# Optimization experiments

Measured on AMD Instinct MI355X. Metric: run time of the kernel, lower is better.

## Reference

```python
import jax, jax.numpy as jnp
import numpy as np

B, S, H, A, O = 512, 64, 1024, 1024, 1024
ATT = 64  # attention logit width (== encoder seq len)


def setup_inputs() -> dict:
    key = jax.random.key(0)
    ks = jax.random.split(key, 14)
    s = lambda *sh: 1.0 / np.sqrt(sh[-1])
    return {
        "encoder_outputs": jax.random.normal(ks[0], (B, S, A), jnp.float32),
        "hidden": jax.random.normal(ks[1], (1, B, H), jnp.float32),
        "max_length": 128,
        # attention: Linear(H+O -> 64)
        "Wa": jax.random.normal(ks[2], (ATT, H + O), jnp.float32) * s(H + O),
        "ba": jnp.zeros((ATT,), jnp.float32),
        # attention_combine: Linear(A+O -> H)
        "Wc": jax.random.normal(ks[3], (H, A + O), jnp.float32) * s(A + O),
        "bc": jnp.zeros((H,), jnp.float32),
        # GRU (1 layer): weight_ih [3H,H], weight_hh [3H,H]
        "W_ih": jax.random.normal(ks[4], (3 * H, H), jnp.float32) * s(H),
        "W_hh": jax.random.normal(ks[5], (3 * H, H), jnp.float32) * s(H),
        "b_ih": jnp.zeros((3 * H,), jnp.float32),
        "b_hh": jnp.zeros((3 * H,), jnp.float32),
        # fc_out: Linear(H -> O)
        "Wo": jax.random.normal(ks[6], (O, H), jnp.float32) * s(H),
        "bo": jnp.zeros((O,), jnp.float32),
    }


def _decode(encoder_outputs, h0, max_length, Wa, ba, Wc, bc, W_ih, W_hh, b_ih, b_hh, Wo, bo):
    Hs = h0.shape[-1]
    dec0 = jnp.zeros((encoder_outputs.shape[0], Wo.shape[0]), encoder_outputs.dtype)

    def step(carry, _):
        dec_in, h = carry  # [B,O], [B,H]
        temp = jnp.concatenate([dec_in, h], axis=1)  # [B, O+H]... matches cat(dec, hidden[-1])
        attn_w = jax.nn.softmax(temp @ Wa.T + ba, axis=1)  # [B,64]
        attn_applied = jnp.einsum("bs,bsd->bd", attn_w, encoder_outputs)  # [B,A]
        gru_in = jax.nn.relu(jnp.concatenate([dec_in, attn_applied], axis=1) @ Wc.T + bc)  # [B,H]
        # single-step PyTorch GRU cell
        gi = gru_in @ W_ih.T + b_ih  # [B,3H]
        gh = h @ W_hh.T + b_hh
        r = jax.nn.sigmoid(gi[:, :Hs] + gh[:, :Hs])
        z = jax.nn.sigmoid(gi[:, Hs:2 * Hs] + gh[:, Hs:2 * Hs])
        n = jnp.tanh(gi[:, 2 * Hs:] + r * gh[:, 2 * Hs:])
        h_new = (1.0 - z) * n + z * h
        out_tok = h_new @ Wo.T + bo  # [B,O]
        return (out_tok, h_new), out_tok

    (_, h_fin), outs = jax.lax.scan(step, (dec0, h0[0]), None, length=max_length)
    output_seq = jnp.transpose(outs, (1, 0, 2))  # [B,T,O]
    return output_seq, h_fin[None]


def reference(encoder_outputs, hidden, max_length, Wa, ba, Wc, bc, W_ih, W_hh, b_ih, b_hh, Wo, bo):
    return _decode(encoder_outputs, hidden, max_length, Wa, ba, Wc, bc, W_ih, W_hh, b_ih, b_hh, Wo, bo)
```

## Files before the change

### kernel.cpp

```cpp
#include <hip/hip_runtime.h>
#include <hip/hip_bf16.h>

#define B 512
#define S 64
#define H 1024
#define O 1024
#define T 128
#define ATT 64

typedef __bf16 bf16;
typedef __bf16 bf16x8 __attribute__((ext_vector_type(8)));
typedef __bf16 bf16x4 __attribute__((ext_vector_type(4)));
typedef float f32x4 __attribute__((ext_vector_type(4)));

static __device__ __forceinline__ float bf2f(bf16 b) {
    unsigned short s = __builtin_bit_cast(unsigned short, b);
    unsigned int u = ((unsigned int)s) << 16;
    return __builtin_bit_cast(float, u);
}
static __device__ __forceinline__ bf16 f2bf(float f) {
    unsigned int u = __builtin_bit_cast(unsigned int, f);
    unsigned int r = (u + 0x7fffu + ((u >> 16) & 1u)) >> 16;
    return __builtin_bit_cast(bf16, (unsigned short)r);
}

template <bool RELU, int K, int SPLITK, int KSTART>
__global__ __launch_bounds__(256) void gemm_kernel(
    const bf16* __restrict__ A0, long lda0,
    const bf16* __restrict__ A1, long lda1,
    const bf16* __restrict__ W, const float* __restrict__ bias,
    float* __restrict__ Cf, long ldc, bf16* __restrict__ Cbf, int ldcbf) {
    const int tid = threadIdx.x;
    const int wave = tid >> 6, lane = tid & 63;
    const int wm = wave >> 1, wn = wave & 1;
    const int quad = lane >> 4, r = lane & 15;
    const int kq = quad * 8;

    const int m0 = blockIdx.y * 32 + wm * 16 + r;
    const int n0 = blockIdx.x * 64 + wn * 32;

    const bf16* a0row = A0 + (long)m0 * lda0;
    const bf16* a1row = A1 + (long)m0 * lda1;
    const bf16* w0 = W + (long)(n0 + r) * K;
    const bf16* w1 = W + (long)(n0 + 16 + r) * K;

    f32x4 acc0 = {0.f, 0.f, 0.f, 0.f}, acc1 = {0.f, 0.f, 0.f, 0.f};

    for (int k0 = KSTART; k0 < K; k0 += 32) {
        bf16x8 av;
        if (k0 < SPLITK)
            av = *(const bf16x8*)(a0row + k0 + kq);
        else
            av = *(const bf16x8*)(a1row + (k0 - SPLITK) + kq);
        bf16x8 bv0 = *(const bf16x8*)(w0 + k0 + kq);
        bf16x8 bv1 = *(const bf16x8*)(w1 + k0 + kq);
        acc0 = __builtin_amdgcn_mfma_f32_16x16x32_bf16(av, bv0, acc0, 0, 0, 0);
        acc1 = __builtin_amdgcn_mfma_f32_16x16x32_bf16(av, bv1, acc1, 0, 0, 0);
    }

    const int mbase = blockIdx.y * 32 + wm * 16 + quad * 4;
    const int nA = n0 + r, nB = n0 + 16 + r;
    const float biasA = bias[nA], biasB = bias[nB];
#pragma unroll
    for (int reg = 0; reg < 4; ++reg) {
        const int m = mbase + reg;
        float vA = acc0[reg] + biasA;
        float vB = acc1[reg] + biasB;
        if (RELU) { vA = fmaxf(vA, 0.f); vB = fmaxf(vB, 0.f); }
        if (Cf) {
            Cf[(long)m * ldc + nA] = vA;
            Cf[(long)m * ldc + nB] = vB;
        }
        if (Cbf) {
            Cbf[(long)m * ldcbf + nA] = f2bf(vA);
            Cbf[(long)m * ldcbf + nB] = f2bf(vB);
        }
    }
}

__global__ __launch_bounds__(256) void fcout_batch_kernel(
    const bf16* __restrict__ Hh, const bf16* __restrict__ Wo,
    const float* __restrict__ bo, float* __restrict__ out) {
    const int tid = threadIdx.x;
    const int wave = tid >> 6, lane = tid & 63;
    const int wm = wave >> 1, wn = wave & 1;
    const int quad = lane >> 4, r = lane & 15;
    const int kq = quad * 8;

    const int m0 = blockIdx.y * 32 + wm * 16 + r;
    const int n0 = blockIdx.x * 64 + wn * 32;

    const bf16* arow = Hh + (long)m0 * H;
    const bf16* w0 = Wo + (long)(n0 + r) * H;
    const bf16* w1 = Wo + (long)(n0 + 16 + r) * H;

    f32x4 acc0 = {0.f, 0.f, 0.f, 0.f}, acc1 = {0.f, 0.f, 0.f, 0.f};
    for (int k0 = 0; k0 < H; k0 += 32) {
        bf16x8 av = *(const bf16x8*)(arow + k0 + kq);
        bf16x8 bv0 = *(const bf16x8*)(w0 + k0 + kq);
        bf16x8 bv1 = *(const bf16x8*)(w1 + k0 + kq);
        acc0 = __builtin_amdgcn_mfma_f32_16x16x32_bf16(av, bv0, acc0, 0, 0, 0);
        acc1 = __builtin_amdgcn_mfma_f32_16x16x32_bf16(av, bv1, acc1, 0, 0, 0);
    }

    const int mbase = blockIdx.y * 32 + wm * 16 + quad * 4;
    const int nA = n0 + r, nB = n0 + 16 + r;
    const float biasA = bo[nA], biasB = bo[nB];
#pragma unroll
    for (int reg = 0; reg < 4; ++reg) {
        const int m = mbase + reg;
        const int b = m & (B - 1);
        const int tt = m >> 9;
        float* orow = out + (long)b * ((long)T * O) + (long)tt * O;
        orow[nA] = acc0[reg] + biasA;
        orow[nB] = acc1[reg] + biasB;
    }
}

__global__ __launch_bounds__(256) void attn_logits_kernel(
    const bf16* __restrict__ h, const bf16* __restrict__ Wlog,
    const float* __restrict__ bvec, bf16* __restrict__ attn_w) {
    __shared__ float lg[32][64];
    const int tid = threadIdx.x;
    const int wave = tid >> 6, lane = tid & 63;
    const int wm = wave >> 1, wn = wave & 1;
    const int quad = lane >> 4, r = lane & 15;
    const int kq = quad * 8;

    const int m0 = blockIdx.y * 32 + wm * 16 + r;
    const int n0 = wn * 32;

    const bf16* hrow = h + (long)m0 * H;
    const bf16* w0 = Wlog + (long)(n0 + r) * H;
    const bf16* w1 = Wlog + (long)(n0 + 16 + r) * H;

    f32x4 acc0 = {0.f, 0.f, 0.f, 0.f}, acc1 = {0.f, 0.f, 0.f, 0.f};
    for (int k0 = 0; k0 < H; k0 += 32) {
        bf16x8 av = *(const bf16x8*)(hrow + k0 + kq);
        bf16x8 bv0 = *(const bf16x8*)(w0 + k0 + kq);
        bf16x8 bv1 = *(const bf16x8*)(w1 + k0 + kq);
        acc0 = __builtin_amdgcn_mfma_f32_16x16x32_bf16(av, bv0, acc0, 0, 0, 0);
        acc1 = __builtin_amdgcn_mfma_f32_16x16x32_bf16(av, bv1, acc1, 0, 0, 0);
    }

    const int mloc = wm * 16 + quad * 4;
#pragma unroll
    for (int reg = 0; reg < 4; ++reg) {
        lg[mloc + reg][n0 + r] = acc0[reg] + bvec[n0 + r];
        lg[mloc + reg][n0 + 16 + r] = acc1[reg] + bvec[n0 + 16 + r];
    }
    __syncthreads();

    if (tid < 32) {
        const int row = tid;
        float mx = -1e30f;
#pragma unroll
        for (int s = 0; s < 64; ++s) mx = fmaxf(mx, lg[row][s]);
        float sum = 0.f;
#pragma unroll
        for (int s = 0; s < 64; ++s) sum += __expf(lg[row][s] - mx);
        const float inv = 1.f / sum;
        const long gb = (long)(blockIdx.y * 32 + row) * 64;
#pragma unroll
        for (int s = 0; s < 64; ++s)
            attn_w[gb + s] = f2bf(__expf(lg[row][s] - mx) * inv);
    }
}

__global__ __launch_bounds__(256) void attn_apply_kernel(
    const bf16* __restrict__ attn_w, const bf16* __restrict__ enc,
    bf16* __restrict__ attn_out) {
    __shared__ float w[64];
    const int b = blockIdx.x;
    const int tid = threadIdx.x;
    if (tid < 64) w[tid] = bf2f(attn_w[b * 64 + tid]);
    __syncthreads();
    const bf16* e = enc + (long)b * (S * 1024) + tid * 4;
    float a0 = 0.f, a1 = 0.f, a2 = 0.f, a3 = 0.f;
#pragma unroll 16
    for (int s = 0; s < S; ++s) {
        unsigned long long raw =
            __builtin_nontemporal_load((const unsigned long long*)(e + (long)s * 1024));
        bf16x4 v = __builtin_bit_cast(bf16x4, raw);
        const float ws = w[s];
        a0 += ws * bf2f(v[0]);
        a1 += ws * bf2f(v[1]);
        a2 += ws * bf2f(v[2]);
        a3 += ws * bf2f(v[3]);
    }
    bf16x4 o = {f2bf(a0), f2bf(a1), f2bf(a2), f2bf(a3)};
    *(bf16x4*)(attn_out + (long)b * 1024 + tid * 4) = o;
}

__global__ __launch_bounds__(256) void gru_kernel(
    const bf16* __restrict__ gin, const bf16* __restrict__ hbf,
    const bf16* __restrict__ Wih, const bf16* __restrict__ Whh,
    const float* __restrict__ bih, const float* __restrict__ bhh,
    const float* __restrict__ hold, float* __restrict__ hnew,
    bf16* __restrict__ hnewbf) {
    const int tid = threadIdx.x;
    const int wave = tid >> 6, lane = tid & 63;
    const int wm = wave >> 1, wn = wave & 1;
    const int quad = lane >> 4, r = lane & 15;
    const int kq = quad * 8;

    const int m0 = blockIdx.y * 32 + wm * 16 + r;
    const int n0 = blockIdx.x * 64 + wn * 32;

    const bf16* grow = gin + (long)m0 * H;
    const bf16* hrow = hbf + (long)m0 * H;

    const bf16* wi[3][2];
    const bf16* wh[3][2];
#pragma unroll
    for (int g = 0; g < 3; ++g) {
#pragma unroll
        for (int ni = 0; ni < 2; ++ni) {
            const long row = (long)g * H + n0 + ni * 16 + r;
            wi[g][ni] = Wih + row * H;
            wh[g][ni] = Whh + row * H;
        }
    }

    f32x4 aI[3][2], aH[3][2];
#pragma unroll
    for (int g = 0; g < 3; ++g)
#pragma unroll
        for (int ni = 0; ni < 2; ++ni) {
            aI[g][ni] = (f32x4){0.f, 0.f, 0.f, 0.f};
            aH[g][ni] = (f32x4){0.f, 0.f, 0.f, 0.f};
        }

    for (int k0 = 0; k0 < H; k0 += 32) {
        const int ko = k0 + kq;
        bf16x8 ai = *(const bf16x8*)(grow + ko);
        bf16x8 ah = *(const bf16x8*)(hrow + ko);
#pragma unroll
        for (int g = 0; g < 3; ++g) {
#pragma unroll
            for (int ni = 0; ni < 2; ++ni) {
                bf16x8 bi = *(const bf16x8*)(wi[g][ni] + ko);
                aI[g][ni] = __builtin_amdgcn_mfma_f32_16x16x32_bf16(ai, bi, aI[g][ni], 0, 0, 0);
                bf16x8 bh = *(const bf16x8*)(wh[g][ni] + ko);
                aH[g][ni] = __builtin_amdgcn_mfma_f32_16x16x32_bf16(ah, bh, aH[g][ni], 0, 0, 0);
            }
        }
    }

    const int mbase = blockIdx.y * 32 + wm * 16 + quad * 4;
#pragma unroll
    for (int ni = 0; ni < 2; ++ni) {
        const int j = n0 + ni * 16 + r;
        const float bir = bih[j], biz = bih[j + H], bin = bih[j + 2 * H];
        const float bhr = bhh[j], bhz = bhh[j + H], bhn = bhh[j + 2 * H];
#pragma unroll
        for (int reg = 0; reg < 4; ++reg) {
            const int m = mbase + reg;
            const float gir = aI[0][ni][reg] + bir, ghr = aH[0][ni][reg] + bhr;
            const float giz = aI[1][ni][reg] + biz, ghz = aH[1][ni][reg] + bhz;
            const float ginv = aI[2][ni][reg] + bin, ghn = aH[2][ni][reg] + bhn;
            const float rg = 1.f / (1.f + __expf(-(gir + ghr)));
            const float zg = 1.f / (1.f + __expf(-(giz + ghz)));
            const float ng = tanhf(ginv + rg * ghn);
            const long idx = (long)m * H + j;
            const float hv = hold[idx];
            const float hnv = (1.f - zg) * ng + zg * hv;
            hnew[idx] = hnv;
            hnewbf[idx] = f2bf(hnv);
        }
    }
}

__global__ __launch_bounds__(256) void cast2d_kernel(
    const float* __restrict__ src, long ld_src, long soff,
    bf16* __restrict__ dst, long ld_dst, long doff, long rows, long cols4) {
    const long total = rows * cols4;
    const long stride = (long)gridDim.x * blockDim.x;
    for (long i = (long)blockIdx.x * blockDim.x + threadIdx.x; i < total; i += stride) {
        const long rr = i / cols4;
        const long c = (i - rr * cols4) << 2;
        const float4 v = *(const float4*)(src + rr * ld_src + soff + c);
        bf16x4 o = {f2bf(v.x), f2bf(v.y), f2bf(v.z), f2bf(v.w)};
        *(bf16x4*)(dst + rr * ld_dst + doff + c) = o;
    }
}

__global__ __launch_bounds__(256) void transpose_cast_kernel(
    const float* __restrict__ src, bf16* __restrict__ dst, int n) {
    __shared__ float tile[32][33];
    const int tx = threadIdx.x & 31, ty = threadIdx.x >> 5;
    const int x0 = blockIdx.x * 32, y0 = blockIdx.y * 32;
#pragma unroll
    for (int i = 0; i < 32; i += 8)
        tile[ty + i][tx] = src[(long)(y0 + ty + i) * n + x0 + tx];
    __syncthreads();
#pragma unroll
    for (int i = 0; i < 32; i += 8)
        dst[(long)(x0 + ty + i) * n + y0 + tx] = f2bf(tile[tx][ty + i]);
}

__global__ __launch_bounds__(256) void addcast_wlog_kernel(
    const float* __restrict__ P1, const float* __restrict__ Wa,
    bf16* __restrict__ Wlog1) {
    const int i = blockIdx.x * 256 + threadIdx.x;
    if (i < 64 * 1024) {
        const int rr = i >> 10, c = i & 1023;
        Wlog1[i] = f2bf(P1[i] + Wa[(long)rr * 2048 + 1024 + c]);
    }
}

__global__ __launch_bounds__(256) void bias_fuse_kernel(
    const float* __restrict__ W, long ld, const float* __restrict__ v,
    const float* __restrict__ b_in, float* __restrict__ b_out) {
    __shared__ float red[256];
    const int r = blockIdx.x, tid = threadIdx.x;
    float s = 0.f;
    for (int j = tid; j < 1024; j += 256) s += W[(long)r * ld + j] * v[j];
    red[tid] = s;
    __syncthreads();
    for (int off = 128; off > 0; off >>= 1) {
        if (tid < off) red[tid] += red[tid + off];
        __syncthreads();
    }
    if (tid == 0) b_out[r] = b_in[r] + red[0];
}

__global__ __launch_bounds__(256) void init_h_kernel(
    const float* __restrict__ h0, float* __restrict__ hfp,
    bf16* __restrict__ hbf, long n4) {
    long i = (long)blockIdx.x * blockDim.x + threadIdx.x;
    const long stride = (long)gridDim.x * blockDim.x;
    for (; i < n4; i += stride) {
        float4 v = ((const float4*)h0)[i];
        ((float4*)hfp)[i] = v;
        bf16x4 o = {f2bf(v.x), f2bf(v.y), f2bf(v.z), f2bf(v.w)};
        *(bf16x4*)(hbf + 4 * i) = o;
    }
}

__global__ __launch_bounds__(256) void copy_f32_kernel(
    const float* __restrict__ src, float* __restrict__ dst, long n4) {
    long i = (long)blockIdx.x * blockDim.x + threadIdx.x;
    const long stride = (long)gridDim.x * blockDim.x;
    for (; i < n4; i += stride) ((float4*)dst)[i] = ((const float4*)src)[i];
}

extern "C" void kernel_launch(void* const* d_in, const int* in_sizes, int n_in,
                              void* d_out, int out_size, void* d_ws, size_t ws_size,
                              hipStream_t stream) {
    const float* enc_f = (const float*)d_in[0];
    const float* hidden = (const float*)d_in[1];
    const float* Wa = (const float*)d_in[3];
    const float* ba = (const float*)d_in[4];
    const float* Wc = (const float*)d_in[5];
    const float* bc = (const float*)d_in[6];
    const float* Wih = (const float*)d_in[7];
    const float* Whh = (const float*)d_in[8];
    const float* bih = (const float*)d_in[9];
    const float* bhh = (const float*)d_in[10];
    const float* Wo = (const float*)d_in[11];
    const float* bo = (const float*)d_in[12];
    float* out = (float*)d_out;

    char* p = (char*)d_ws;
    auto carve = [&](long bytes) {
        char* q = p;
        p += (bytes + 255) & ~255L;
        return q;
    };
    bf16* Wlog0 = (bf16*)carve((long)64 * 1024 * 2);
    bf16* Wlog1 = (bf16*)carve((long)64 * 1024 * 2);
    bf16* Wcomb = (bf16*)carve((long)H * 2048 * 2);
    bf16* Wih_bf = (bf16*)carve((long)3 * H * H * 2);
    bf16* Whh_bf = (bf16*)carve((long)3 * H * H * 2);
    bf16* Wo_bf = (bf16*)carve((long)O * H * 2);
    bf16* enc_bf = (bf16*)carve((long)B * S * 1024 * 2);
    bf16* attn_bf = (bf16*)carve((long)B * 1024 * 2);
    bf16* gru_bf = (bf16*)carve((long)B * H * 2);
    bf16* attn_w = (bf16*)carve((long)B * 64 * 2);
    bf16* h0bf = (bf16*)carve((long)B * H * 2);
    bf16* hbfA = (bf16*)carve((long)B * H * 2);
    bf16* hbfB = (bf16*)carve((long)B * H * 2);
    float* hfpA = (float*)carve((long)B * H * 4);
    float* hfpB = (float*)carve((long)B * H * 4);
    float* blog1 = (float*)carve(64 * 4);
    float* bc2 = (float*)carve((long)H * 4);
    float* zeros = (float*)carve(1024 * 4);

    const long persistent = (long)(p - (char*)d_ws);
    const long histBytes = (long)T * B * H * 2;
    const bool batched = (ws_size >= (size_t)(persistent + histBytes + 256));
    bf16* hist = batched ? (bf16*)carve(histBytes) : nullptr;
    auto slot = [&](int t2) -> bf16* {
        return batched ? hist + (long)t2 * ((long)B * H)
                       : ((t2 & 1) ? hbfB : hbfA);
    };

    {
        char* sp = (char*)enc_bf;
        auto scarve = [&](long bytes) {
            char* q = sp;
            sp += (bytes + 255) & ~255L;
            return q;
        };
        bf16* Wad = (bf16*)scarve((long)64 * 1024 * 2);
        bf16* Wcd = (bf16*)scarve((long)H * 1024 * 2);
        bf16* WoT = (bf16*)scarve((long)H * O * 2);
        float* P1 = (float*)scarve((long)64 * 1024 * 4);
        float* P2 = (float*)scarve((long)H * 1024 * 4);

        hipMemsetAsync(zeros, 0, 1024 * 4, stream);

        auto cast2d = [&](const float* src, long lds_, long so, bf16* dst,
                          long ldd, long doff, long rows, long cols) {
            long n4 = rows * (cols / 4);
            int blocks = (int)((n4 + 255) / 256);
            if (blocks > 4096) blocks = 4096;
            cast2d_kernel<<<blocks, 256, 0, stream>>>(src, lds_, so, dst, ldd,
                                                      doff, rows, cols / 4);
        };
        cast2d(Wa, 2048, 1024, Wlog0, 1024, 0, 64, 1024);
        cast2d(Wa, 2048, 0, Wad, 1024, 0, 64, 1024);
        cast2d(Wc, 2048, 0, Wcd, 1024, 0, 1024, 1024);
        cast2d(Wc, 2048, 1024, Wcomb, 2048, 1024, 1024, 1024);
        cast2d(Wih, 1024, 0, Wih_bf, 1024, 0, 3 * H, 1024);
        cast2d(Whh, 1024, 0, Whh_bf, 1024, 0, 3 * H, 1024);
        cast2d(Wo, 1024, 0, Wo_bf, 1024, 0, O, 1024);
        transpose_cast_kernel<<<dim3(32, 32), 256, 0, stream>>>(Wo, WoT, 1024);

        gemm_kernel<false, 1024, 1024, 0><<<dim3(16, 2), 256, 0, stream>>>(
            Wad, 1024, Wad, 1024, WoT, zeros, P1, 1024, nullptr, 0);
        gemm_kernel<false, 1024, 1024, 0><<<dim3(16, 32), 256, 0, stream>>>(
            Wcd, 1024, Wcd, 1024, WoT, zeros, P2, 1024, nullptr, 0);

        addcast_wlog_kernel<<<256, 256, 0, stream>>>(P1, Wa, Wlog1);
        cast2d(P2, 1024, 0, Wcomb, 2048, 0, 1024, 1024);

        bias_fuse_kernel<<<64, 256, 0, stream>>>(Wa, 2048, bo, ba, blog1);
        bias_fuse_kernel<<<1024, 256, 0, stream>>>(Wc, 2048, bo, bc, bc2);

        cast2d(enc_f, 1024, 0, enc_bf, 1024, 0, (long)B * S, 1024);
        init_h_kernel<<<512, 256, 0, stream>>>(hidden, hfpA, h0bf, (long)B * H / 4);
    }

    const dim3 blk(256);
    const dim3 grid_nm(H / 64, B / 32);
    const dim3 grid_attn(1, B / 32);

    for (int t = 0; t < T; ++t) {
        const bf16* h_in = (t == 0) ? h0bf : slot(t - 1);
        bf16* h_out = slot(t);
        const float* hfp_r = (t & 1) ? hfpB : hfpA;
        float* hfp_w = (t & 1) ? hfpA : hfpB;

        attn_logits_kernel<<<grid_attn, blk, 0, stream>>>(
            h_in, t ? Wlog1 : Wlog0, t ? blog1 : ba, attn_w);
        attn_apply_kernel<<<B, blk, 0, stream>>>(attn_w, enc_bf, attn_bf);
        if (t == 0)
            gemm_kernel<true, 2048, 1024, 1024><<<grid_nm, blk, 0, stream>>>(
                h_in, 1024, attn_bf, 1024, Wcomb, bc, nullptr, 0, gru_bf, H);
        else
            gemm_kernel<true, 2048, 1024, 0><<<grid_nm, blk, 0, stream>>>(
                h_in, 1024, attn_bf, 1024, Wcomb, bc2, nullptr, 0, gru_bf, H);
        gru_kernel<<<grid_nm, blk, 0, stream>>>(
            gru_bf, h_in, Wih_bf, Whh_bf, bih, bhh, hfp_r, hfp_w, h_out);
        if (!batched)
            gemm_kernel<false, 1024, 1024, 0><<<grid_nm, blk, 0, stream>>>(
                h_out, 1024, h_out, 1024, Wo_bf, bo,
                out + (long)t * O, (long)T * O, nullptr, 0);
    }

    if (batched)
        fcout_batch_kernel<<<dim3(16, (T * B) / 32), blk, 0, stream>>>(
            hist, Wo_bf, bo, out);

    copy_f32_kernel<<<512, 256, 0, stream>>>(hfpA, out + (long)B * T * O,
                                             (long)B * H / 4);
}
```

Baseline: 15.48 ms.

## Fuse attention logits/softmax into apply kernel and halve GEMM/GRU tile width

Merges the attention-logit GEMM plus softmax into the per-batch attention-apply kernel. Each block now computes its 64 logits with scalar dot products from an LDS-staged hidden row, which removes one launch and the attn_w round trip per step. The combine GEMM and GRU kernels drop from 64 to 32 output columns per block, doubling the grid to 512 blocks to raise occupancy on the many CUs. In exchange, A-row reloads increase and each block does less MFMA work per load.

```diff
diff --git a/kernel.cpp b/kernel.cpp
--- a/kernel.cpp
+++ b/kernel.cpp
@@ -78,6 +78,50 @@
     }
 }
 
+template <bool RELU, int K, int SPLITK, int KSTART>
+__global__ __launch_bounds__(256) void gemm32_kernel(
+    const bf16* __restrict__ A0, long lda0,
+    const bf16* __restrict__ A1, long lda1,
+    const bf16* __restrict__ W, const float* __restrict__ bias,
+    float* __restrict__ Cf, long ldc, bf16* __restrict__ Cbf, int ldcbf) {
+    const int tid = threadIdx.x;
+    const int wave = tid >> 6, lane = tid & 63;
+    const int wm = wave >> 1, wn = wave & 1;
+    const int quad = lane >> 4, r = lane & 15;
+    const int kq = quad * 8;
+
+    const int m0 = blockIdx.y * 32 + wm * 16 + r;
+    const int n0 = blockIdx.x * 32 + wn * 16;
+
+    const bf16* a0row = A0 + (long)m0 * lda0;
+    const bf16* a1row = A1 + (long)m0 * lda1;
+    const bf16* w0 = W + (long)(n0 + r) * K;
+
+    f32x4 acc0 = {0.f, 0.f, 0.f, 0.f};
+
+    for (int k0 = KSTART; k0 < K; k0 += 32) {
+        bf16x8 av;
+        if (k0 < SPLITK)
+            av = *(const bf16x8*)(a0row + k0 + kq);
+        else
+            av = *(const bf16x8*)(a1row + (k0 - SPLITK) + kq);
+        bf16x8 bv0 = *(const bf16x8*)(w0 + k0 + kq);
+        acc0 = __builtin_amdgcn_mfma_f32_16x16x32_bf16(av, bv0, acc0, 0, 0, 0);
+    }
+
+    const int mbase = blockIdx.y * 32 + wm * 16 + quad * 4;
+    const int nA = n0 + r;
+    const float biasA = bias[nA];
+#pragma unroll
+    for (int reg = 0; reg < 4; ++reg) {
+        const int m = mbase + reg;
+        float vA = acc0[reg] + biasA;
+        if (RELU) vA = fmaxf(vA, 0.f);
+        if (Cf) Cf[(long)m * ldc + nA] = vA;
+        if (Cbf) Cbf[(long)m * ldcbf + nA] = f2bf(vA);
+    }
+}
+
 __global__ __launch_bounds__(256) void fcout_batch_kernel(
     const bf16* __restrict__ Hh, const bf16* __restrict__ Wo,
     const float* __restrict__ bo, float* __restrict__ out) {
@@ -117,72 +161,67 @@
     }
 }
 
-__global__ __launch_bounds__(256) void attn_logits_kernel(
+#define HIDX(k) ((k) + (((k) >> 8) << 2))
+__global__ __launch_bounds__(256) void attn_fused_kernel(
     const bf16* __restrict__ h, const bf16* __restrict__ Wlog,
-    const float* __restrict__ bvec, bf16* __restrict__ attn_w) {
-    __shared__ float lg[32][64];
-    const int tid = threadIdx.x;
-    const int wave = tid >> 6, lane = tid & 63;
-    const int wm = wave >> 1, wn = wave & 1;
-    const int quad = lane >> 4, r = lane & 15;
-    const int kq = quad * 8;
-
-    const int m0 = blockIdx.y * 32 + wm * 16 + r;
-    const int n0 = wn * 32;
-
-    const bf16* hrow = h + (long)m0 * H;
-    const bf16* w0 = Wlog + (long)(n0 + r) * H;
-    const bf16* w1 = Wlog + (long)(n0 + 16 + r) * H;
-
-    f32x4 acc0 = {0.f, 0.f, 0.f, 0.f}, acc1 = {0.f, 0.f, 0.f, 0.f};
-    for (int k0 = 0; k0 < H; k0 += 32) {
-        bf16x8 av = *(const bf16x8*)(hrow + k0 + kq);
-        bf16x8 bv0 = *(const bf16x8*)(w0 + k0 + kq);
-        bf16x8 bv1 = *(const bf16x8*)(w1 + k0 + kq);
-        acc0 = __builtin_amdgcn_mfma_f32_16x16x32_bf16(av, bv0, acc0, 0, 0, 0);
-        acc1 = __builtin_amdgcn_mfma_f32_16x16x32_bf16(av, bv1, acc1, 0, 0, 0);
-    }
-
-    const int mloc = wm * 16 + quad * 4;
-#pragma unroll
-    for (int reg = 0; reg < 4; ++reg) {
-        lg[mloc + reg][n0 + r] = acc0[reg] + bvec[n0 + r];
-        lg[mloc + reg][n0 + 16 + r] = acc1[reg] + bvec[n0 + 16 + r];
-    }
-    __syncthreads();
-
-    if (tid < 32) {
-        const int row = tid;
-        float mx = -1e30f;
-#pragma unroll
-        for (int s = 0; s < 64; ++s) mx = fmaxf(mx, lg[row][s]);
-        float sum = 0.f;
-#pragma unroll
-        for (int s = 0; s < 64; ++s) sum += __expf(lg[row][s] - mx);
-        const float inv = 1.f / sum;
-        const long gb = (long)(blockIdx.y * 32 + row) * 64;
-#pragma unroll
-        for (int s = 0; s < 64; ++s)
-            attn_w[gb + s] = f2bf(__expf(lg[row][s] - mx) * inv);
-    }
-}
-
-__global__ __launch_bounds__(256) void attn_apply_kernel(
-    const bf16* __restrict__ attn_w, const bf16* __restrict__ enc,
+    const float* __restrict__ bvec, const bf16* __restrict__ enc,
     bf16* __restrict__ attn_out) {
-    __shared__ float w[64];
+    __shared__ float hsh[1040];
+    __shared__ float lg[64];
+    __shared__ float wbuf[64];
     const int b = blockIdx.x;
     const int tid = threadIdx.x;
-    if (tid < 64) w[tid] = bf2f(attn_w[b * 64 + tid]);
+
+    {
+        const int k = tid * 4;
+        bf16x4 v = *(const bf16x4*)(h + (long)b * H + k);
+        float4 f = {bf2f(v[0]), bf2f(v[1]), bf2f(v[2]), bf2f(v[3])};
+        *(float4*)&hsh[HIDX(k)] = f;
+    }
     __syncthreads();
+
+    {
+        const int s = tid >> 2, kpart = tid & 3;
+        const bf16* wrow = Wlog + (long)s * 1024 + kpart * 256;
+        const int kb = kpart * 256;
+        float acc = 0.f;
+#pragma unroll
+        for (int i = 0; i < 32; ++i) {
+            bf16x8 wv = *(const bf16x8*)(wrow + i * 8);
+            const float4 ha = *(const float4*)&hsh[HIDX(kb + i * 8)];
+            const float4 hb = *(const float4*)&hsh[HIDX(kb + i * 8 + 4)];
+            acc += bf2f(wv[0]) * ha.x + bf2f(wv[1]) * ha.y +
+                   bf2f(wv[2]) * ha.z + bf2f(wv[3]) * ha.w +
+                   bf2f(wv[4]) * hb.x + bf2f(wv[5]) * hb.y +
+                   bf2f(wv[6]) * hb.z + bf2f(wv[7]) * hb.w;
+        }
+        acc += __shfl_xor(acc, 1);
+        acc += __shfl_xor(acc, 2);
+        if (kpart == 0) lg[s] = acc + bvec[s];
+    }
+    __syncthreads();
+
+    if (tid < 64) {
+        const float v = lg[tid];
+        float mx = v;
+#pragma unroll
+        for (int off = 32; off; off >>= 1) mx = fmaxf(mx, __shfl_xor(mx, off));
+        const float e = __expf(v - mx);
+        float sum = e;
+#pragma unroll
+        for (int off = 32; off; off >>= 1) sum += __shfl_xor(sum, off);
+        wbuf[tid] = e / sum;
+    }
+    __syncthreads();
+
     const bf16* e = enc + (long)b * (S * 1024) + tid * 4;
     float a0 = 0.f, a1 = 0.f, a2 = 0.f, a3 = 0.f;
 #pragma unroll 16
-    for (int s = 0; s < S; ++s) {
+    for (int s2 = 0; s2 < S; ++s2) {
         unsigned long long raw =
-            __builtin_nontemporal_load((const unsigned long long*)(e + (long)s * 1024));
+            __builtin_nontemporal_load((const unsigned long long*)(e + (long)s2 * 1024));
         bf16x4 v = __builtin_bit_cast(bf16x4, raw);
-        const float ws = w[s];
+        const float ws = wbuf[s2];
         a0 += ws * bf2f(v[0]);
         a1 += ws * bf2f(v[1]);
         a2 += ws * bf2f(v[2]);
@@ -192,7 +231,7 @@
     *(bf16x4*)(attn_out + (long)b * 1024 + tid * 4) = o;
 }
 
-__global__ __launch_bounds__(256) void gru_kernel(
+__global__ __launch_bounds__(256) void gru32_kernel(
     const bf16* __restrict__ gin, const bf16* __restrict__ hbf,
     const bf16* __restrict__ Wih, const bf16* __restrict__ Whh,
     const float* __restrict__ bih, const float* __restrict__ bhh,
@@ -205,31 +244,26 @@
     const int kq = quad * 8;
 
     const int m0 = blockIdx.y * 32 + wm * 16 + r;
-    const int n0 = blockIdx.x * 64 + wn * 32;
+    const int n0 = blockIdx.x * 32 + wn * 16;
 
     const bf16* grow = gin + (long)m0 * H;
     const bf16* hrow = hbf + (long)m0 * H;
 
-    const bf16* wi[3][2];
-    const bf16* wh[3][2];
+    const bf16* wi[3];
+    const bf16* wh[3];
 #pragma unroll
     for (int g = 0; g < 3; ++g) {
-#pragma unroll
-        for (int ni = 0; ni < 2; ++ni) {
-            const long row = (long)g * H + n0 + ni * 16 + r;
-            wi[g][ni] = Wih + row * H;
-            wh[g][ni] = Whh + row * H;
-        }
-    }
-
-    f32x4 aI[3][2], aH[3][2];
-#pragma unroll
-    for (int g = 0; g < 3; ++g)
-#pragma unroll
-        for (int ni = 0; ni < 2; ++ni) {
-            aI[g][ni] = (f32x4){0.f, 0.f, 0.f, 0.f};
-            aH[g][ni] = (f32x4){0.f, 0.f, 0.f, 0.f};
-        }
+        const long row = (long)g * H + n0 + r;
+        wi[g] = Wih + row * H;
+        wh[g] = Whh + row * H;
+    }
+
+    f32x4 aI[3], aH[3];
+#pragma unroll
+    for (int g = 0; g < 3; ++g) {
+        aI[g] = (f32x4){0.f, 0.f, 0.f, 0.f};
+        aH[g] = (f32x4){0.f, 0.f, 0.f, 0.f};
+    }
 
     for (int k0 = 0; k0 < H; k0 += 32) {
         const int ko = k0 + kq;
@@ -237,37 +271,31 @@
         bf16x8 ah = *(const bf16x8*)(hrow + ko);
 #pragma unroll
         for (int g = 0; g < 3; ++g) {
-#pragma unroll
-            for (int ni = 0; ni < 2; ++ni) {
-                bf16x8 bi = *(const bf16x8*)(wi[g][ni] + ko);
-                aI[g][ni] = __builtin_amdgcn_mfma_f32_16x16x32_bf16(ai, bi, aI[g][ni], 0, 0, 0);
-                bf16x8 bh = *(const bf16x8*)(wh[g][ni] + ko);
-                aH[g][ni] = __builtin_amdgcn_mfma_f32_16x16x32_bf16(ah, bh, aH[g][ni], 0, 0, 0);
-            }
+            bf16x8 bi = *(const bf16x8*)(wi[g] + ko);
+            aI[g] = __builtin_amdgcn_mfma_f32_16x16x32_bf16(ai, bi, aI[g], 0, 0, 0);
+            bf16x8 bh = *(const bf16x8*)(wh[g] + ko);
+            aH[g] = __builtin_amdgcn_mfma_f32_16x16x32_bf16(ah, bh, aH[g], 0, 0, 0);
         }
     }
 
     const int mbase = blockIdx.y * 32 + wm * 16 + quad * 4;
-#pragma unroll
-    for (int ni = 0; ni < 2; ++ni) {
-        const int j = n0 + ni * 16 + r;
-        const float bir = bih[j], biz = bih[j + H], bin = bih[j + 2 * H];
-        const float bhr = bhh[j], bhz = bhh[j + H], bhn = bhh[j + 2 * H];
-#pragma unroll
-        for (int reg = 0; reg < 4; ++reg) {
-            const int m = mbase + reg;
-            const float gir = aI[0][ni][reg] + bir, ghr = aH[0][ni][reg] + bhr;
-            const float giz = aI[1][ni][reg] + biz, ghz = aH[1][ni][reg] + bhz;
-            const float ginv = aI[2][ni][reg] + bin, ghn = aH[2][ni][reg] + bhn;
-            const float rg = 1.f / (1.f + __expf(-(gir + ghr)));
-            const float zg = 1.f / (1.f + __expf(-(giz + ghz)));
-            const float ng = tanhf(ginv + rg * ghn);
-            const long idx = (long)m * H + j;
-            const float hv = hold[idx];
-            const float hnv = (1.f - zg) * ng + zg * hv;
-            hnew[idx] = hnv;
-            hnewbf[idx] = f2bf(hnv);
-        }
+    const int j = n0 + r;
+    const float bir = bih[j], biz = bih[j + H], bin = bih[j + 2 * H];
+    const float bhr = bhh[j], bhz = bhh[j + H], bhn = bhh[j + 2 * H];
+#pragma unroll
+    for (int reg = 0; reg < 4; ++reg) {
+        const int m = mbase + reg;
+        const float gir = aI[0][reg] + bir, ghr = aH[0][reg] + bhr;
+        const float giz = aI[1][reg] + biz, ghz = aH[1][reg] + bhz;
+        const float ginv = aI[2][reg] + bin, ghn = aH[2][reg] + bhn;
+        const float rg = 1.f / (1.f + __expf(-(gir + ghr)));
+        const float zg = 1.f / (1.f + __expf(-(giz + ghz)));
+        const float ng = tanhf(ginv + rg * ghn);
+        const long idx = (long)m * H + j;
+        const float hv = hold[idx];
+        const float hnv = (1.f - zg) * ng + zg * hv;
+        hnew[idx] = hnv;
+        hnewbf[idx] = f2bf(hnv);
     }
 }
 
@@ -377,7 +405,6 @@
     bf16* enc_bf = (bf16*)carve((long)B * S * 1024 * 2);
     bf16* attn_bf = (bf16*)carve((long)B * 1024 * 2);
     bf16* gru_bf = (bf16*)carve((long)B * H * 2);
-    bf16* attn_w = (bf16*)carve((long)B * 64 * 2);
     bf16* h0bf = (bf16*)carve((long)B * H * 2);
     bf16* hbfA = (bf16*)carve((long)B * H * 2);
     bf16* hbfB = (bf16*)carve((long)B * H * 2);
@@ -444,8 +471,8 @@
     }
 
     const dim3 blk(256);
-    const dim3 grid_nm(H / 64, B / 32);
-    const dim3 grid_attn(1, B / 32);
+    const dim3 grid32(H / 32, B / 32);
+    const dim3 grid64(H / 64, B / 32);
 
     for (int t = 0; t < T; ++t) {
         const bf16* h_in = (t == 0) ? h0bf : slot(t - 1);
@@ -453,19 +480,18 @@
         const float* hfp_r = (t & 1) ? hfpB : hfpA;
         float* hfp_w = (t & 1) ? hfpA : hfpB;
 
-        attn_logits_kernel<<<grid_attn, blk, 0, stream>>>(
-            h_in, t ? Wlog1 : Wlog0, t ? blog1 : ba, attn_w);
-        attn_apply_kernel<<<B, blk, 0, stream>>>(attn_w, enc_bf, attn_bf);
+        attn_fused_kernel<<<B, blk, 0, stream>>>(
+            h_in, t ? Wlog1 : Wlog0, t ? blog1 : ba, enc_bf, attn_bf);
         if (t == 0)
-            gemm_kernel<true, 2048, 1024, 1024><<<grid_nm, blk, 0, stream>>>(
+            gemm32_kernel<true, 2048, 1024, 1024><<<grid32, blk, 0, stream>>>(
                 h_in, 1024, attn_bf, 1024, Wcomb, bc, nullptr, 0, gru_bf, H);
         else
-            gemm_kernel<true, 2048, 1024, 0><<<grid_nm, blk, 0, stream>>>(
+            gemm32_kernel<true, 2048, 1024, 0><<<grid32, blk, 0, stream>>>(
                 h_in, 1024, attn_bf, 1024, Wcomb, bc2, nullptr, 0, gru_bf, H);
-        gru_kernel<<<grid_nm, blk, 0, stream>>>(
+        gru32_kernel<<<grid32, blk, 0, stream>>>(
             gru_bf, h_in, Wih_bf, Whh_bf, bih, bhh, hfp_r, hfp_w, h_out);
         if (!batched)
-            gemm_kernel<false, 1024, 1024, 0><<<grid_nm, blk, 0, stream>>>(
+            gemm_kernel<false, 1024, 1024, 0><<<grid64, blk, 0, stream>>>(
                 h_out, 1024, h_out, 1024, Wo_bf, bo,
                 out + (long)t * O, (long)T * O, nullptr, 0);
     }
```

New measurement: 16.00 ms. 3.3% more time.
